# Kernel tuning notes

Hardware: AMD Instinct MI355X
Metric: run time of the kernel (lower is better)

Reference implementation:

```python
import jax, jax.numpy as jnp
import numpy as np
from jax import lax

PATCH = 16          # patch_size
LAM = 0.5           # lambda_sparse
TAU = 10.0          # tau
ITERS = 50          # lca_iterations
DT = 0.1            # LCA step size
N_BASES = 256
INPUT_DIM = PATCH * PATCH * 3


def setup_inputs() -> dict:
    key = jax.random.key(0)
    k1, k2 = jax.random.split(key)
    image = jax.random.normal(k1, (64, 3, 224, 224), dtype=jnp.float32)
    D = jax.random.normal(k2, (N_BASES, INPUT_DIM), dtype=jnp.float32)
    D = D / jnp.linalg.norm(D, axis=1, keepdims=True)  # unit-norm bases
    return {"image": image, "dictionary": D, "stride": 8}


def _softshrink(u):
    return jnp.sign(u) * jnp.maximum(jnp.abs(u) - LAM, 0.0)


def reference(image, dictionary, stride):
    n_bases = dictionary.shape[0]
    # extract overlapping patches, feature order (C, ph, pw) matches torch unfold layout
    patches = lax.conv_general_dilated_patches(
        image, (PATCH, PATCH), (stride, stride), 'VALID')  # (B, C*P*P, nh, nw)
    B, D, nh, nw = patches.shape
    patches = patches.transpose(0, 2, 3, 1).reshape(B, nh * nw, D)
    # per-patch standardization (torch .std is unbiased -> ddof=1)
    patches = patches - patches.mean(axis=-1, keepdims=True)
    std = jnp.std(patches, axis=-1, ddof=1, keepdims=True)
    patches = patches / (std + 1e-8)

    pf = patches.reshape(-1, D)  # (B*n_patches, input_dim)
    gram = dictionary @ dictionary.T - jnp.eye(n_bases, dtype=dictionary.dtype)
    b = pf @ dictionary.T        # (N, n_bases) feedforward drive

    def step(u, _):
        a = _softshrink(u)
        du = (b - u - a @ gram) / TAU
        return u + DT * du, None

    u0 = jnp.zeros_like(b)
    u, _ = lax.scan(step, u0, None, length=ITERS)
    codes = _softshrink(u).reshape(B, nh * nw, n_bases)
    return codes.max(axis=1)  # pool='max' -> (B, n_bases)
```

## Files before the change

kernel.cpp:

```cpp
#include <hip/hip_runtime.h>
#include <hip/hip_bf16.h>

#define NB 256
#define IDIM 768
#define NPP 729
#define PSTRIDE 768
#define NIMG 64
#define ITERS 50
#define LN 32
#define LBLK 24

typedef float f32x4 __attribute__((ext_vector_type(4)));
typedef short bf16x8 __attribute__((ext_vector_type(8)));

__device__ __forceinline__ short f2bf(float x) {
  union { float f; unsigned u; } v; v.f = x;
  unsigned r = v.u + 0x7FFFu + ((v.u >> 16) & 1u);
  return (short)(r >> 16);
}

__device__ __forceinline__ float bf2f(short s) {
  return __uint_as_float((unsigned)(unsigned short)s << 16);
}

__device__ __forceinline__ unsigned cvt_pk_bf16(float lo, float hi) {
  unsigned r;
  asm("v_cvt_pk_bf16_f32 %0, %1, %2" : "=v"(r) : "v"(lo), "v"(hi));
  return r;
}

__global__ __launch_bounds__(256) void k_cvt(const float* __restrict__ D,
                                             short* __restrict__ Dbf) {
  size_t i = (size_t)(blockIdx.x * 256 + threadIdx.x) * 8;
  float4 a = *(const float4*)(D + i);
  float4 b = *(const float4*)(D + i + 4);
  union { uint4 u4; bf16x8 v; } cv;
  cv.u4.x = cvt_pk_bf16(a.x, a.y); cv.u4.y = cvt_pk_bf16(a.z, a.w);
  cv.u4.z = cvt_pk_bf16(b.x, b.y); cv.u4.w = cvt_pk_bf16(b.z, b.w);
  *(bf16x8*)(Dbf + i) = cv.v;
}

__global__ __launch_bounds__(256) void k_dsum(const short* __restrict__ Dbf,
                                              float* __restrict__ dsum) {
  int j = threadIdx.x;
  float s = 0.f;
  for (int kc = 0; kc < 96; ++kc) {
    bf16x8 v = *(const bf16x8*)(Dbf + (size_t)j * IDIM + kc * 8);
    #pragma unroll
    for (int i = 0; i < 8; ++i) s += bf2f(v[i]);
  }
  dsum[j] = s;
}

__global__ __launch_bounds__(256) void k_gram(const short* __restrict__ Dbf,
                                              short* __restrict__ gram) {
  int r0 = blockIdx.x * 16;
  int t = threadIdx.x, w = t >> 6, l = t & 63, lr = l & 15, q = l >> 4;
  f32x4 acc[4];
  #pragma unroll
  for (int c = 0; c < 4; ++c) acc[c] = (f32x4){0.f, 0.f, 0.f, 0.f};
  for (int kc = 0; kc < 24; ++kc) {
    int k = kc * 32 + q * 8;
    bf16x8 a = *(const bf16x8*)(Dbf + (size_t)(r0 + lr) * IDIM + k);
    #pragma unroll
    for (int c = 0; c < 4; ++c) {
      int col = (w * 4 + c) * 16 + lr;
      bf16x8 b = *(const bf16x8*)(Dbf + (size_t)col * IDIM + k);
      acc[c] = __builtin_amdgcn_mfma_f32_16x16x32_bf16(a, b, acc[c], 0, 0, 0);
    }
  }
  #pragma unroll
  for (int c = 0; c < 4; ++c)
    #pragma unroll
    for (int r = 0; r < 4; ++r) {
      int row = r0 + q * 4 + r, col = (w * 4 + c) * 16 + lr;
      gram[row * NB + col] = f2bf(acc[c][r] - (row == col ? 1.f : 0.f));
    }
}

__global__ __launch_bounds__(256) void k_patches(const float* __restrict__ img,
                                                 const short* __restrict__ Dbf,
                                                 const float* __restrict__ dsum,
                                                 float* __restrict__ bbufT) {
  __shared__ float strip[3 * 16 * 224];
  __shared__ float s_mean[32], s_inv[32];
  int py = blockIdx.x, im = blockIdx.y;
  int t = threadIdx.x;

  for (int i = t; i < 2688; i += 256) {
    int c = i / 896, rem = i - c * 896, ph = rem / 56, x = rem - ph * 56;
    float4 v = *(const float4*)(img + ((size_t)(im * 3 + c)) * 50176 +
                                (size_t)(py * 8 + ph) * 224 + x * 4);
    *(float4*)(strip + (c * 16 + ph) * 224 + x * 4) = v;
  }
  if (t >= 216 && t < 221) { s_mean[27 + t - 216] = 0.f; s_inv[27 + t - 216] = 0.f; }
  __syncthreads();
  if (t < 216) {
    int p = t >> 3, s = t & 7;
    float sum = 0.f, ss = 0.f;
    for (int c = 0; c < 3; ++c)
      #pragma unroll
      for (int ph = 0; ph < 16; ++ph) {
        const float* rw = strip + (c * 16 + ph) * 224 + p * 8 + s * 2;
        float v0 = rw[0], v1 = rw[1];
        sum += v0 + v1; ss += v0 * v0 + v1 * v1;
      }
    #pragma unroll
    for (int d = 1; d < 8; d <<= 1) { sum += __shfl_xor(sum, d); ss += __shfl_xor(ss, d); }
    if (s == 0) {
      float mean = sum * (1.f / 768.f);
      float var = (ss - sum * mean) * (1.f / 767.f);
      float sd = sqrtf(fmaxf(var, 0.f));
      s_mean[p] = mean; s_inv[p] = 1.f / (sd + 1e-8f);
    }
  }
  __syncthreads();

  int w = t >> 6, l = t & 63, lr = l & 15, q = l >> 4;
  f32x4 acc[2][4];
  #pragma unroll
  for (int mi = 0; mi < 2; ++mi)
    #pragma unroll
    for (int c = 0; c < 4; ++c) acc[mi][c] = (f32x4){0.f, 0.f, 0.f, 0.f};

  for (int kc = 0; kc < 24; ++kc) {
    int k = kc * 32 + q * 8;
    int c = k >> 8, ph = (k >> 4) & 15, pw0 = k & 15;
    const float* rb = strip + (c * 16 + ph) * 224 + pw0;
    bf16x8 af[2];
    #pragma unroll
    for (int mi = 0; mi < 2; ++mi) {
      int patch = mi * 16 + lr;
      int px = patch < 27 ? patch : 26;
      const float* sp = rb + px * 8;
      float4 v0 = *(const float4*)(sp);
      float4 v1 = *(const float4*)(sp + 4);
      union { uint4 u4; bf16x8 v; } cv;
      cv.u4.x = cvt_pk_bf16(v0.x, v0.y);
      cv.u4.y = cvt_pk_bf16(v0.z, v0.w);
      cv.u4.z = cvt_pk_bf16(v1.x, v1.y);
      cv.u4.w = cvt_pk_bf16(v1.z, v1.w);
      af[mi] = cv.v;
    }
    bf16x8 bfr[4];
    #pragma unroll
    for (int c4 = 0; c4 < 4; ++c4) {
      int col = (w * 4 + c4) * 16 + lr;
      bfr[c4] = *(const bf16x8*)(Dbf + (size_t)col * IDIM + k);
    }
    #pragma unroll
    for (int mi = 0; mi < 2; ++mi)
      #pragma unroll
      for (int c4 = 0; c4 < 4; ++c4)
        acc[mi][c4] = __builtin_amdgcn_mfma_f32_16x16x32_bf16(af[mi], bfr[c4], acc[mi][c4], 0, 0, 0);
  }

  int prow0 = py * 27;
  #pragma unroll
  for (int mi = 0; mi < 2; ++mi)
    #pragma unroll
    for (int c4 = 0; c4 < 4; ++c4) {
      int col = (w * 4 + c4) * 16 + lr;
      float dsv = dsum[col];
      size_t base = ((size_t)(im * NB + col)) * PSTRIDE + prow0;
      #pragma unroll
      for (int r = 0; r < 4; ++r) {
        int patch = mi * 16 + q * 4 + r;
        if (patch < 27) {
          float bv = (acc[mi][c4][r] - s_mean[patch] * dsv) * s_inv[patch];
          bbufT[base + patch] = bv;
        }
      }
    }
}

__global__ __launch_bounds__(256, 2) void k_lca(const float* __restrict__ bbufT,
                                                const short* __restrict__ gram,
                                                float* __restrict__ partial) {
  __shared__ char albuf[2][LN * 512];
  int blk = blockIdx.x, im = blockIdx.y;
  int t = threadIdx.x, w = t >> 6, l = t & 63, lr = l & 15, q = l >> 4;
  int p0 = blk * LN;
  int basew = w * 64;

  bf16x8 gA[4][8];
  #pragma unroll
  for (int mi = 0; mi < 4; ++mi)
    #pragma unroll
    for (int kc = 0; kc < 8; ++kc)
      gA[mi][kc] = *(const bf16x8*)(gram + (size_t)(basew + mi * 16 + lr) * NB + kc * 32 + q * 8);

  float u[4][2][4];
  int2 bpk[4][2];
  #pragma unroll
  for (int mi = 0; mi < 4; ++mi) {
    int basis0 = basew + mi * 16 + q * 4;
    #pragma unroll
    for (int nt = 0; nt < 2; ++nt) {
      int patch = nt * 16 + lr;
      size_t ga = ((size_t)(im * NB + basis0)) * PSTRIDE + p0 + patch;
      float b0 = bbufT[ga] * 0.01f;
      float b1 = bbufT[ga + PSTRIDE] * 0.01f;
      float b2 = bbufT[ga + 2 * PSTRIDE] * 0.01f;
      float b3 = bbufT[ga + 3 * PSTRIDE] * 0.01f;
      int2 pk = make_int2((int)cvt_pk_bf16(b0, b1), (int)cvt_pk_bf16(b2, b3));
      bpk[mi][nt] = pk;
      u[mi][nt][0] = __uint_as_float((unsigned)pk.x << 16);
      u[mi][nt][1] = __uint_as_float((unsigned)pk.x & 0xffff0000u);
      u[mi][nt][2] = __uint_as_float((unsigned)pk.y << 16);
      u[mi][nt][3] = __uint_as_float((unsigned)pk.y & 0xffff0000u);
    }
  }

  for (int it = 0; it < ITERS - 1; ++it) {
    char* abuf = albuf[it & 1];
    #pragma unroll
    for (int mi = 0; mi < 4; ++mi)
      #pragma unroll
      for (int nt = 0; nt < 2; ++nt) {
        int patch = nt * 16 + lr;
        float a0 = u[mi][nt][0] - __builtin_amdgcn_fmed3f(u[mi][nt][0], -0.5f, 0.5f);
        float a1 = u[mi][nt][1] - __builtin_amdgcn_fmed3f(u[mi][nt][1], -0.5f, 0.5f);
        float a2 = u[mi][nt][2] - __builtin_amdgcn_fmed3f(u[mi][nt][2], -0.5f, 0.5f);
        float a3 = u[mi][nt][3] - __builtin_amdgcn_fmed3f(u[mi][nt][3], -0.5f, 0.5f);
        int byte = (patch * 512 + (basew + mi * 16 + q * 4) * 2) ^ ((patch & 7) << 4);
        *(int2*)(abuf + byte) = make_int2((int)cvt_pk_bf16(a0, a1), (int)cvt_pk_bf16(a2, a3));
      }
    __syncthreads();

    f32x4 acc[4][2];
    #pragma unroll
    for (int mi = 0; mi < 4; ++mi)
      #pragma unroll
      for (int nt = 0; nt < 2; ++nt) acc[mi][nt] = (f32x4){0.f, 0.f, 0.f, 0.f};
    #pragma unroll
    for (int kc = 0; kc < 8; ++kc) {
      bf16x8 ab[2];
      #pragma unroll
      for (int nt = 0; nt < 2; ++nt) {
        int patch = nt * 16 + lr;
        int byte = (patch * 512 + (kc * 32 + q * 8) * 2) ^ ((patch & 7) << 4);
        ab[nt] = *(const bf16x8*)(abuf + byte);
      }
      #pragma unroll
      for (int mi = 0; mi < 4; ++mi)
        #pragma unroll
        for (int nt = 0; nt < 2; ++nt)
          acc[mi][nt] = __builtin_amdgcn_mfma_f32_16x16x32_bf16(gA[mi][kc], ab[nt], acc[mi][nt], 0, 0, 0);
    }

    #pragma unroll
    for (int mi = 0; mi < 4; ++mi)
      #pragma unroll
      for (int nt = 0; nt < 2; ++nt) {
        int2 pk = bpk[mi][nt];
        float b0 = __uint_as_float((unsigned)pk.x << 16);
        float b1 = __uint_as_float((unsigned)pk.x & 0xffff0000u);
        float b2 = __uint_as_float((unsigned)pk.y << 16);
        float b3 = __uint_as_float((unsigned)pk.y & 0xffff0000u);
        u[mi][nt][0] = fmaf(0.99f, u[mi][nt][0], fmaf(-0.01f, acc[mi][nt][0], b0));
        u[mi][nt][1] = fmaf(0.99f, u[mi][nt][1], fmaf(-0.01f, acc[mi][nt][1], b1));
        u[mi][nt][2] = fmaf(0.99f, u[mi][nt][2], fmaf(-0.01f, acc[mi][nt][2], b2));
        u[mi][nt][3] = fmaf(0.99f, u[mi][nt][3], fmaf(-0.01f, acc[mi][nt][3], b3));
      }
  }

  #pragma unroll
  for (int mi = 0; mi < 4; ++mi)
    #pragma unroll
    for (int r = 0; r < 4; ++r) {
      float m = -3.402823466e38f;
      #pragma unroll
      for (int nt = 0; nt < 2; ++nt) {
        int patch = p0 + nt * 16 + lr;
        float uu = u[mi][nt][r];
        float a = uu - __builtin_amdgcn_fmed3f(uu, -0.5f, 0.5f);
        if (patch < NPP) m = fmaxf(m, a);
      }
      m = fmaxf(m, __shfl_xor(m, 1));
      m = fmaxf(m, __shfl_xor(m, 2));
      m = fmaxf(m, __shfl_xor(m, 4));
      m = fmaxf(m, __shfl_xor(m, 8));
      if (lr == 0)
        partial[(size_t)(im * LBLK + blk) * NB + basew + mi * 16 + q * 4 + r] = m;
    }
}

__global__ __launch_bounds__(256) void k_pool(const float* __restrict__ partial,
                                              float* __restrict__ out) {
  int im = blockIdx.x, n = threadIdx.x;
  float m = partial[(size_t)(im * LBLK) * NB + n];
  for (int b = 1; b < LBLK; ++b)
    m = fmaxf(m, partial[(size_t)(im * LBLK + b) * NB + n]);
  out[im * NB + n] = m;
}

extern "C" void kernel_launch(void* const* d_in, const int* in_sizes, int n_in,
                              void* d_out, int out_size, void* d_ws, size_t ws_size,
                              hipStream_t stream) {
  const float* img = (const float*)d_in[0];
  const float* D   = (const float*)d_in[1];

  char* ws = (char*)d_ws;
  short* gram    = (short*)(ws);
  short* Dbf     = (short*)(ws + 131072);
  float* dsum    = (float*)(ws + 524288);
  float* bbufT   = (float*)(ws + 528384);
  float* partial = (float*)(ws + 50860032);
  float* out = (float*)d_out;

  hipLaunchKernelGGL(k_cvt, dim3(96), dim3(256), 0, stream, D, Dbf);
  hipLaunchKernelGGL(k_dsum, dim3(1), dim3(256), 0, stream, Dbf, dsum);
  hipLaunchKernelGGL(k_gram, dim3(16), dim3(256), 0, stream, Dbf, gram);
  hipLaunchKernelGGL(k_patches, dim3(27, NIMG), dim3(256), 0, stream, img, Dbf, dsum, bbufT);
  hipLaunchKernelGGL(k_lca, dim3(LBLK, NIMG), dim3(256), 0, stream, bbufT, gram, partial);
  hipLaunchKernelGGL(k_pool, dim3(NIMG), dim3(256), 0, stream, partial, out);
}
```

Baseline: 432.0 us.

## Switch LCA loop to 32x32x16 MFMA with 8 waves per block

Restructures the LCA iteration kernel so each of 8 waves (512 threads) owns 32 bases times 32 patches and uses a single 32x32x16 bf16 MFMA chain instead of 4x2 tiles of 16x16x32. The gram slice held in registers per wave drops from 64 to 32 rows, which frees registers and allows higher occupancy. The change also trims the patch-row padding (PSTRIDE 768 to 736, LBLK 24 to 23) to avoid a wasted block. Trade-offs: a longer dependent MFMA chain per wave and a block-wide barrier across more waves each iteration.

```diff
diff --git a/kernel.cpp b/kernel.cpp
--- a/kernel.cpp
+++ b/kernel.cpp
@@ -4,13 +4,14 @@
 #define NB 256
 #define IDIM 768
 #define NPP 729
-#define PSTRIDE 768
+#define PSTRIDE 736
 #define NIMG 64
 #define ITERS 50
 #define LN 32
-#define LBLK 24
+#define LBLK 23
 
 typedef float f32x4 __attribute__((ext_vector_type(4)));
+typedef float f32x16 __attribute__((ext_vector_type(16)));
 typedef short bf16x8 __attribute__((ext_vector_type(8)));
 
 __device__ __forceinline__ short f2bf(float x) {
@@ -174,115 +175,91 @@
     }
 }
 
-__global__ __launch_bounds__(256, 2) void k_lca(const float* __restrict__ bbufT,
+__global__ __launch_bounds__(512, 4) void k_lca(const float* __restrict__ bbufT,
                                                 const short* __restrict__ gram,
                                                 float* __restrict__ partial) {
   __shared__ char albuf[2][LN * 512];
   int blk = blockIdx.x, im = blockIdx.y;
-  int t = threadIdx.x, w = t >> 6, l = t & 63, lr = l & 15, q = l >> 4;
+  int t = threadIdx.x, w = t >> 6, l = t & 63;
+  int p = l & 31, hi = l >> 5;
   int p0 = blk * LN;
-  int basew = w * 64;
-
-  bf16x8 gA[4][8];
-  #pragma unroll
-  for (int mi = 0; mi < 4; ++mi)
-    #pragma unroll
-    for (int kc = 0; kc < 8; ++kc)
-      gA[mi][kc] = *(const bf16x8*)(gram + (size_t)(basew + mi * 16 + lr) * NB + kc * 32 + q * 8);
-
-  float u[4][2][4];
-  int2 bpk[4][2];
-  #pragma unroll
-  for (int mi = 0; mi < 4; ++mi) {
-    int basis0 = basew + mi * 16 + q * 4;
-    #pragma unroll
-    for (int nt = 0; nt < 2; ++nt) {
-      int patch = nt * 16 + lr;
-      size_t ga = ((size_t)(im * NB + basis0)) * PSTRIDE + p0 + patch;
-      float b0 = bbufT[ga] * 0.01f;
-      float b1 = bbufT[ga + PSTRIDE] * 0.01f;
-      float b2 = bbufT[ga + 2 * PSTRIDE] * 0.01f;
-      float b3 = bbufT[ga + 3 * PSTRIDE] * 0.01f;
-      int2 pk = make_int2((int)cvt_pk_bf16(b0, b1), (int)cvt_pk_bf16(b2, b3));
-      bpk[mi][nt] = pk;
-      u[mi][nt][0] = __uint_as_float((unsigned)pk.x << 16);
-      u[mi][nt][1] = __uint_as_float((unsigned)pk.x & 0xffff0000u);
-      u[mi][nt][2] = __uint_as_float((unsigned)pk.y << 16);
-      u[mi][nt][3] = __uint_as_float((unsigned)pk.y & 0xffff0000u);
-    }
+  int swz = (p & 7) << 4;
+  int p512 = p * 512;
+
+  bf16x8 gA[16];
+  #pragma unroll
+  for (int ks = 0; ks < 16; ++ks)
+    gA[ks] = *(const bf16x8*)(gram + (size_t)(w * 32 + p) * NB + ks * 16 + hi * 8);
+
+  float u[16];
+  int2 bpk[4];
+  #pragma unroll
+  for (int g = 0; g < 4; ++g) {
+    int basis0 = w * 32 + g * 8 + hi * 4;
+    size_t ga = ((size_t)(im * NB + basis0)) * PSTRIDE + p0 + p;
+    float b0 = bbufT[ga] * 0.01f;
+    float b1 = bbufT[ga + PSTRIDE] * 0.01f;
+    float b2 = bbufT[ga + 2 * PSTRIDE] * 0.01f;
+    float b3 = bbufT[ga + 3 * PSTRIDE] * 0.01f;
+    int2 pk = make_int2((int)cvt_pk_bf16(b0, b1), (int)cvt_pk_bf16(b2, b3));
+    bpk[g] = pk;
+    u[4 * g + 0] = __uint_as_float((unsigned)pk.x << 16);
+    u[4 * g + 1] = __uint_as_float((unsigned)pk.x & 0xffff0000u);
+    u[4 * g + 2] = __uint_as_float((unsigned)pk.y << 16);
+    u[4 * g + 3] = __uint_as_float((unsigned)pk.y & 0xffff0000u);
   }
 
   for (int it = 0; it < ITERS - 1; ++it) {
     char* abuf = albuf[it & 1];
     #pragma unroll
-    for (int mi = 0; mi < 4; ++mi)
-      #pragma unroll
-      for (int nt = 0; nt < 2; ++nt) {
-        int patch = nt * 16 + lr;
-        float a0 = u[mi][nt][0] - __builtin_amdgcn_fmed3f(u[mi][nt][0], -0.5f, 0.5f);
-        float a1 = u[mi][nt][1] - __builtin_amdgcn_fmed3f(u[mi][nt][1], -0.5f, 0.5f);
-        float a2 = u[mi][nt][2] - __builtin_amdgcn_fmed3f(u[mi][nt][2], -0.5f, 0.5f);
-        float a3 = u[mi][nt][3] - __builtin_amdgcn_fmed3f(u[mi][nt][3], -0.5f, 0.5f);
-        int byte = (patch * 512 + (basew + mi * 16 + q * 4) * 2) ^ ((patch & 7) << 4);
-        *(int2*)(abuf + byte) = make_int2((int)cvt_pk_bf16(a0, a1), (int)cvt_pk_bf16(a2, a3));
-      }
+    for (int g = 0; g < 4; ++g) {
+      float a0 = u[4 * g + 0] - __builtin_amdgcn_fmed3f(u[4 * g + 0], -0.5f, 0.5f);
+      float a1 = u[4 * g + 1] - __builtin_amdgcn_fmed3f(u[4 * g + 1], -0.5f, 0.5f);
+      float a2 = u[4 * g + 2] - __builtin_amdgcn_fmed3f(u[4 * g + 2], -0.5f, 0.5f);
+      float a3 = u[4 * g + 3] - __builtin_amdgcn_fmed3f(u[4 * g + 3], -0.5f, 0.5f);
+      int byte = (p512 + w * 64 + g * 16 + hi * 8) ^ swz;
+      *(int2*)(abuf + byte) = make_int2((int)cvt_pk_bf16(a0, a1), (int)cvt_pk_bf16(a2, a3));
+    }
     __syncthreads();
 
-    f32x4 acc[4][2];
-    #pragma unroll
-    for (int mi = 0; mi < 4; ++mi)
-      #pragma unroll
-      for (int nt = 0; nt < 2; ++nt) acc[mi][nt] = (f32x4){0.f, 0.f, 0.f, 0.f};
-    #pragma unroll
-    for (int kc = 0; kc < 8; ++kc) {
-      bf16x8 ab[2];
-      #pragma unroll
-      for (int nt = 0; nt < 2; ++nt) {
-        int patch = nt * 16 + lr;
-        int byte = (patch * 512 + (kc * 32 + q * 8) * 2) ^ ((patch & 7) << 4);
-        ab[nt] = *(const bf16x8*)(abuf + byte);
-      }
-      #pragma unroll
-      for (int mi = 0; mi < 4; ++mi)
-        #pragma unroll
-        for (int nt = 0; nt < 2; ++nt)
-          acc[mi][nt] = __builtin_amdgcn_mfma_f32_16x16x32_bf16(gA[mi][kc], ab[nt], acc[mi][nt], 0, 0, 0);
-    }
-
-    #pragma unroll
-    for (int mi = 0; mi < 4; ++mi)
-      #pragma unroll
-      for (int nt = 0; nt < 2; ++nt) {
-        int2 pk = bpk[mi][nt];
-        float b0 = __uint_as_float((unsigned)pk.x << 16);
-        float b1 = __uint_as_float((unsigned)pk.x & 0xffff0000u);
-        float b2 = __uint_as_float((unsigned)pk.y << 16);
-        float b3 = __uint_as_float((unsigned)pk.y & 0xffff0000u);
-        u[mi][nt][0] = fmaf(0.99f, u[mi][nt][0], fmaf(-0.01f, acc[mi][nt][0], b0));
-        u[mi][nt][1] = fmaf(0.99f, u[mi][nt][1], fmaf(-0.01f, acc[mi][nt][1], b1));
-        u[mi][nt][2] = fmaf(0.99f, u[mi][nt][2], fmaf(-0.01f, acc[mi][nt][2], b2));
-        u[mi][nt][3] = fmaf(0.99f, u[mi][nt][3], fmaf(-0.01f, acc[mi][nt][3], b3));
-      }
-  }
-
-  #pragma unroll
-  for (int mi = 0; mi < 4; ++mi)
-    #pragma unroll
-    for (int r = 0; r < 4; ++r) {
-      float m = -3.402823466e38f;
-      #pragma unroll
-      for (int nt = 0; nt < 2; ++nt) {
-        int patch = p0 + nt * 16 + lr;
-        float uu = u[mi][nt][r];
-        float a = uu - __builtin_amdgcn_fmed3f(uu, -0.5f, 0.5f);
-        if (patch < NPP) m = fmaxf(m, a);
-      }
+    f32x16 acc;
+    #pragma unroll
+    for (int i = 0; i < 16; ++i) acc[i] = 0.f;
+    #pragma unroll
+    for (int ks = 0; ks < 16; ++ks) {
+      int byte = (p512 + ks * 32 + hi * 16) ^ swz;
+      bf16x8 ab = *(const bf16x8*)(abuf + byte);
+      acc = __builtin_amdgcn_mfma_f32_32x32x16_bf16(gA[ks], ab, acc, 0, 0, 0);
+    }
+
+    #pragma unroll
+    for (int g = 0; g < 4; ++g) {
+      int2 pk = bpk[g];
+      float b0 = __uint_as_float((unsigned)pk.x << 16);
+      float b1 = __uint_as_float((unsigned)pk.x & 0xffff0000u);
+      float b2 = __uint_as_float((unsigned)pk.y << 16);
+      float b3 = __uint_as_float((unsigned)pk.y & 0xffff0000u);
+      u[4 * g + 0] = fmaf(0.99f, u[4 * g + 0], fmaf(-0.01f, acc[4 * g + 0], b0));
+      u[4 * g + 1] = fmaf(0.99f, u[4 * g + 1], fmaf(-0.01f, acc[4 * g + 1], b1));
+      u[4 * g + 2] = fmaf(0.99f, u[4 * g + 2], fmaf(-0.01f, acc[4 * g + 2], b2));
+      u[4 * g + 3] = fmaf(0.99f, u[4 * g + 3], fmaf(-0.01f, acc[4 * g + 3], b3));
+    }
+  }
+
+  #pragma unroll
+  for (int g = 0; g < 4; ++g)
+    #pragma unroll
+    for (int j = 0; j < 4; ++j) {
+      float uu = u[4 * g + j];
+      float a = uu - __builtin_amdgcn_fmed3f(uu, -0.5f, 0.5f);
+      float m = (p0 + p < NPP) ? a : -3.402823466e38f;
       m = fmaxf(m, __shfl_xor(m, 1));
       m = fmaxf(m, __shfl_xor(m, 2));
       m = fmaxf(m, __shfl_xor(m, 4));
       m = fmaxf(m, __shfl_xor(m, 8));
-      if (lr == 0)
-        partial[(size_t)(im * LBLK + blk) * NB + basew + mi * 16 + q * 4 + r] = m;
+      m = fmaxf(m, __shfl_xor(m, 16));
+      if (p == 0)
+        partial[(size_t)(im * LBLK + blk) * NB + w * 32 + g * 8 + hi * 4 + j] = m;
     }
 }
 
@@ -306,13 +283,13 @@
   short* Dbf     = (short*)(ws + 131072);
   float* dsum    = (float*)(ws + 524288);
   float* bbufT   = (float*)(ws + 528384);
-  float* partial = (float*)(ws + 50860032);
+  float* partial = (float*)(ws + 48762880);
   float* out = (float*)d_out;
 
   hipLaunchKernelGGL(k_cvt, dim3(96), dim3(256), 0, stream, D, Dbf);
   hipLaunchKernelGGL(k_dsum, dim3(1), dim3(256), 0, stream, Dbf, dsum);
   hipLaunchKernelGGL(k_gram, dim3(16), dim3(256), 0, stream, Dbf, gram);
   hipLaunchKernelGGL(k_patches, dim3(27, NIMG), dim3(256), 0, stream, img, Dbf, dsum, bbufT);
-  hipLaunchKernelGGL(k_lca, dim3(LBLK, NIMG), dim3(256), 0, stream, bbufT, gram, partial);
+  hipLaunchKernelGGL(k_lca, dim3(LBLK, NIMG), dim3(512), 0, stream, bbufT, gram, partial);
   hipLaunchKernelGGL(k_pool, dim3(NIMG), dim3(256), 0, stream, partial, out);
 }
```

Result: slower. 549.9 us (+27.3%).
